# Optimization experiments

Measured on AMD Instinct MI355X. Metric: run time of the kernel, lower is better.

## Reference

```python
import jax, jax.numpy as jnp
import numpy as np

N = 50000
K = 32
C = 256  # hidden_dim

def setup_inputs() -> dict:
    key = jax.random.key(0)
    k1, k2, k3, k4 = jax.random.split(key, 4)
    feat = jax.random.normal(k1, (N, C), dtype=jnp.float32)
    coords = jax.random.normal(k2, (N, 3), dtype=jnp.float32)
    knn_idx = jax.random.randint(k3, (N, K), 0, N, dtype=jnp.int32)
    # Dense(hidden_dim) over concat([feat(C), agg(C), rel_mean(3), rel_std(3)]) -> in_dim = 2C + 6
    W = jax.random.normal(k4, (2 * C + 6, C), dtype=jnp.float32) * (1.0 / np.sqrt(2 * C + 6))
    b = jnp.zeros((C,), dtype=jnp.float32)
    return {"feat": feat, "coords": coords, "knn_idx": knn_idx, "W": W, "b": b}

def reference(feat, coords, knn_idx, W, b):
    # Neighbor feature aggregation: gather (N,K,C) then mean over K
    nbr_feat = feat[knn_idx]                      # (N, K, C)
    agg = jnp.mean(nbr_feat, axis=1)              # (N, C)
    # Relative coordinate statistics
    nbr_coords = coords[knn_idx]                  # (N, K, 3)
    rel = nbr_coords - coords[:, None, :]         # (N, K, 3)
    rel_mean = jnp.mean(rel, axis=1)              # (N, 3)
    rel_var = jnp.mean(jnp.square(rel), axis=1) - jnp.square(rel_mean)
    rel_std = jnp.sqrt(jnp.maximum(rel_var, 0.0))  # population std, like tf.math.reduce_std
    mix = jnp.concatenate([feat, agg, rel_mean, rel_std], axis=-1)  # (N, 2C+6)
    out = jax.nn.silu(mix @ W + b)                # (N, C)
    return out
```

## Files before the change

kernel.cpp:

```cpp
#include <hip/hip_runtime.h>
#include <math.h>


typedef __attribute__((ext_vector_type(8))) short short8;
typedef __attribute__((ext_vector_type(4))) float f32x4;
typedef __attribute__((ext_vector_type(2))) float f32x2;

constexpr int K = 32;
constexpr int C = 256;
constexpr int IN_DIM = 2 * C + 6;
constexpr int KP = 544;
constexpr int BM = 32;
constexpr int MIXS = 552;
constexpr int NT = 256;

__device__ __forceinline__ unsigned short f2bf(float f) {
  union { float f; unsigned u; } c; c.f = f;
  return (unsigned short)((c.u + 0x7fffu + ((c.u >> 16) & 1u)) >> 16);
}
__device__ __forceinline__ unsigned cvtpk(float lo, float hi) {
  unsigned r;
  asm("v_cvt_pk_bf16_f32 %0, %1, %2" : "=v"(r) : "v"(lo), "v"(hi));
  return r;
}

__global__ __launch_bounds__(256) void prep_feat_q(const float* __restrict__ feat,
                                                   uint2* __restrict__ featq,
                                                   long total8) {
  long i = (long)blockIdx.x * 256 + threadIdx.x;
  if (i < total8) {
    const float4 v0 = reinterpret_cast<const float4*>(feat)[2 * i];
    const float4 v1 = reinterpret_cast<const float4*>(feat)[2 * i + 1];
    unsigned a = 0, b = 0;
    a = __builtin_amdgcn_cvt_pk_fp8_f32(v0.x, v0.y, a, false);
    a = __builtin_amdgcn_cvt_pk_fp8_f32(v0.z, v0.w, a, true);
    b = __builtin_amdgcn_cvt_pk_fp8_f32(v1.x, v1.y, b, false);
    b = __builtin_amdgcn_cvt_pk_fp8_f32(v1.z, v1.w, b, true);
    uint2 o; o.x = a; o.y = b;
    featq[i] = o;
  }
}

__global__ __launch_bounds__(256) void prep_w(const float* __restrict__ W,
                                              unsigned short* __restrict__ Wt) {
  int i = blockIdx.x * 256 + threadIdx.x;
  if (i < C * KP) {
    int nn = i / KP, k = i - nn * KP;
    float v = (k < IN_DIM) ? W[(size_t)k * C + nn] : 0.f;
    if (k >= C && k < 2 * C) v *= (1.0f / 32.0f);
    Wt[i] = f2bf(v);
  }
}

__global__ __launch_bounds__(NT, 4)
void gcl_main(const unsigned char* __restrict__ featq,
              const float* __restrict__ feat,
              const float* __restrict__ coords,
              const int*   __restrict__ knn,
              const unsigned short* __restrict__ Wt,
              const float* __restrict__ bias,
              float* __restrict__ out, int n)
{
  __shared__ unsigned short mix[BM][MIXS];
  __shared__ int knnLds[BM * K];

  const int t = threadIdx.x;
  const int row0 = blockIdx.x * BM;

  #pragma unroll
  for (int i = 0; i < (BM * K) / NT; ++i) {
    int e = t + i * NT;
    int r = e >> 5, k = e & 31;
    int g = row0 + r; if (g >= n) g = n - 1;
    knnLds[e] = knn[(size_t)g * K + k];
  }
  for (int e = t; e < BM * (KP - IN_DIM); e += NT) {
    int r = e / (KP - IN_DIM), c = e - r * (KP - IN_DIM);
    mix[r][IN_DIM + c] = 0;
  }
  __syncthreads();

  const int w    = t >> 6;
  const int lane = t & 63;
  const int cl   = lane & 15;
  const int rq   = lane >> 4;

  #pragma unroll
  for (int p = 0; p < 2; ++p) {
    const int r = (w << 3) + (p << 2) + rq;
    int g = row0 + r; if (g >= n) g = n - 1;

    {
      const float4 s0 = *reinterpret_cast<const float4*>(feat + (size_t)g * C + cl * 16 + 0);
      const float4 s1 = *reinterpret_cast<const float4*>(feat + (size_t)g * C + cl * 16 + 4);
      const float4 s2 = *reinterpret_cast<const float4*>(feat + (size_t)g * C + cl * 16 + 8);
      const float4 s3 = *reinterpret_cast<const float4*>(feat + (size_t)g * C + cl * 16 + 12);
      uint4 o0, o1;
      o0.x = cvtpk(s0.x, s0.y); o0.y = cvtpk(s0.z, s0.w);
      o0.z = cvtpk(s1.x, s1.y); o0.w = cvtpk(s1.z, s1.w);
      o1.x = cvtpk(s2.x, s2.y); o1.y = cvtpk(s2.z, s2.w);
      o1.z = cvtpk(s3.x, s3.y); o1.w = cvtpk(s3.z, s3.w);
      *reinterpret_cast<uint4*>(&mix[r][cl * 16 + 0]) = o0;
      *reinterpret_cast<uint4*>(&mix[r][cl * 16 + 8]) = o1;
    }

    const int* ids = &knnLds[r * K];
    float a0=0,a1=0,a2=0,a3=0,a4=0,a5=0,a6=0,a7=0;
    float a8=0,a9=0,aA=0,aB=0,aC=0,aD=0,aE=0,aF=0;
    #pragma unroll 8
    for (int k = 0; k < K; ++k) {
      const uint4 v = *reinterpret_cast<const uint4*>(featq + (size_t)ids[k] * C + cl * 16);
      f32x2 d0 = __builtin_amdgcn_cvt_pk_f32_fp8(v.x, false);
      f32x2 d1 = __builtin_amdgcn_cvt_pk_f32_fp8(v.x, true);
      f32x2 d2 = __builtin_amdgcn_cvt_pk_f32_fp8(v.y, false);
      f32x2 d3 = __builtin_amdgcn_cvt_pk_f32_fp8(v.y, true);
      f32x2 d4 = __builtin_amdgcn_cvt_pk_f32_fp8(v.z, false);
      f32x2 d5 = __builtin_amdgcn_cvt_pk_f32_fp8(v.z, true);
      f32x2 d6 = __builtin_amdgcn_cvt_pk_f32_fp8(v.w, false);
      f32x2 d7 = __builtin_amdgcn_cvt_pk_f32_fp8(v.w, true);
      a0 += d0.x; a1 += d0.y; a2 += d1.x; a3 += d1.y;
      a4 += d2.x; a5 += d2.y; a6 += d3.x; a7 += d3.y;
      a8 += d4.x; a9 += d4.y; aA += d5.x; aB += d5.y;
      aC += d6.x; aD += d6.y; aE += d7.x; aF += d7.y;
    }
    uint4 o0, o1;
    o0.x = cvtpk(a0, a1); o0.y = cvtpk(a2, a3);
    o0.z = cvtpk(a4, a5); o0.w = cvtpk(a6, a7);
    o1.x = cvtpk(a8, a9); o1.y = cvtpk(aA, aB);
    o1.z = cvtpk(aC, aD); o1.w = cvtpk(aE, aF);
    *reinterpret_cast<uint4*>(&mix[r][C + cl * 16 + 0]) = o0;
    *reinterpret_cast<uint4*>(&mix[r][C + cl * 16 + 8]) = o1;
  }

  #pragma unroll
  for (int pass = 0; pass < 4; ++pass) {
    const int sr = (t >> 5) + pass * 8;
    const int sk = t & 31;
    const int id = knnLds[sr * K + sk];
    const float x = coords[(size_t)id * 3 + 0];
    const float y = coords[(size_t)id * 3 + 1];
    const float z = coords[(size_t)id * 3 + 2];
    float sx = x, sy = y, sz = z;
    float qx = x * x, qy = y * y, qz = z * z;
    #pragma unroll
    for (int m = 1; m < 32; m <<= 1) {
      sx += __shfl_xor(sx, m); sy += __shfl_xor(sy, m); sz += __shfl_xor(sz, m);
      qx += __shfl_xor(qx, m); qy += __shfl_xor(qy, m); qz += __shfl_xor(qz, m);
    }
    if (sk == 0) {
      int g = row0 + sr; if (g >= n) g = n - 1;
      const float inv = 1.0f / 32.0f;
      const float mx = sx * inv, my = sy * inv, mz = sz * inv;
      const float vx = qx * inv - mx * mx;
      const float vy = qy * inv - my * my;
      const float vz = qz * inv - mz * mz;
      mix[sr][2 * C + 0] = f2bf(mx - coords[(size_t)g * 3 + 0]);
      mix[sr][2 * C + 1] = f2bf(my - coords[(size_t)g * 3 + 1]);
      mix[sr][2 * C + 2] = f2bf(mz - coords[(size_t)g * 3 + 2]);
      mix[sr][2 * C + 3] = f2bf(sqrtf(fmaxf(vx, 0.f)));
      mix[sr][2 * C + 4] = f2bf(sqrtf(fmaxf(vy, 0.f)));
      mix[sr][2 * C + 5] = f2bf(sqrtf(fmaxf(vz, 0.f)));
    }
  }
  __syncthreads();

  const int n0  = w * 64;
  const int l15 = lane & 15;
  const int h   = lane >> 4;

  f32x4 acc[2][4];
  #pragma unroll
  for (int mt = 0; mt < 2; ++mt)
    #pragma unroll
    for (int nt = 0; nt < 4; ++nt)
      acc[mt][nt] = (f32x4){0.f, 0.f, 0.f, 0.f};

  const unsigned short* wb = Wt + (size_t)(n0 + l15) * KP + 8 * h;

  short8 B0 = *reinterpret_cast<const short8*>(wb + 0 * 16 * KP);
  short8 B1 = *reinterpret_cast<const short8*>(wb + 1 * 16 * KP);
  short8 B2 = *reinterpret_cast<const short8*>(wb + 2 * 16 * KP);
  short8 B3 = *reinterpret_cast<const short8*>(wb + 3 * 16 * KP);
  short8 A0 = *reinterpret_cast<const short8*>(&mix[l15][8 * h]);
  short8 A1 = *reinterpret_cast<const short8*>(&mix[16 + l15][8 * h]);

  #pragma unroll 1
  for (int s8 = 0; s8 < KP / 32; ++s8) {
    const int kb  = s8 * 32;
    const int kbn = (kb + 32 <= KP - 32) ? kb + 32 : KP - 32;
    short8 nB0 = *reinterpret_cast<const short8*>(wb + 0 * 16 * KP + kbn);
    short8 nB1 = *reinterpret_cast<const short8*>(wb + 1 * 16 * KP + kbn);
    short8 nB2 = *reinterpret_cast<const short8*>(wb + 2 * 16 * KP + kbn);
    short8 nB3 = *reinterpret_cast<const short8*>(wb + 3 * 16 * KP + kbn);
    short8 nA0 = *reinterpret_cast<const short8*>(&mix[l15][kbn + 8 * h]);
    short8 nA1 = *reinterpret_cast<const short8*>(&mix[16 + l15][kbn + 8 * h]);

    acc[0][0] = __builtin_amdgcn_mfma_f32_16x16x32_bf16(A0, B0, acc[0][0], 0, 0, 0);
    acc[1][0] = __builtin_amdgcn_mfma_f32_16x16x32_bf16(A1, B0, acc[1][0], 0, 0, 0);
    acc[0][1] = __builtin_amdgcn_mfma_f32_16x16x32_bf16(A0, B1, acc[0][1], 0, 0, 0);
    acc[1][1] = __builtin_amdgcn_mfma_f32_16x16x32_bf16(A1, B1, acc[1][1], 0, 0, 0);
    acc[0][2] = __builtin_amdgcn_mfma_f32_16x16x32_bf16(A0, B2, acc[0][2], 0, 0, 0);
    acc[1][2] = __builtin_amdgcn_mfma_f32_16x16x32_bf16(A1, B2, acc[1][2], 0, 0, 0);
    acc[0][3] = __builtin_amdgcn_mfma_f32_16x16x32_bf16(A0, B3, acc[0][3], 0, 0, 0);
    acc[1][3] = __builtin_amdgcn_mfma_f32_16x16x32_bf16(A1, B3, acc[1][3], 0, 0, 0);

    B0 = nB0; B1 = nB1; B2 = nB2; B3 = nB3;
    A0 = nA0; A1 = nA1;
  }

  #pragma unroll
  for (int mt = 0; mt < 2; ++mt) {
    #pragma unroll
    for (int nt = 0; nt < 4; ++nt) {
      const int col = n0 + nt * 16 + l15;
      const float bv = bias[col];
      f32x4 a = acc[mt][nt];
      #pragma unroll
      for (int q = 0; q < 4; ++q) {
        const int grow = row0 + mt * 16 + 4 * h + q;
        if (grow < n) {
          const float x = a[q] + bv;
          out[(size_t)grow * C + col] = x * __builtin_amdgcn_rcpf(1.f + __expf(-x));
        }
      }
    }
  }
}

constexpr int BMF = 32;
constexpr int MIX_STRIDE = 520;

#define FMA4(mcomp, wv)                                                        \
  a.x = fmaf((mcomp), (wv).x, a.x);                                            \
  a.y = fmaf((mcomp), (wv).y, a.y);                                            \
  a.z = fmaf((mcomp), (wv).z, a.z);                                            \
  a.w = fmaf((mcomp), (wv).w, a.w);

__global__ __launch_bounds__(256, 2)
void gcl_fused(const float* __restrict__ feat,
               const float* __restrict__ coords,
               const int*   __restrict__ knn,
               const float* __restrict__ W,
               const float* __restrict__ bias,
               float* __restrict__ out,
               int n)
{
  __shared__ float mix[BMF][MIX_STRIDE];
  __shared__ int   knnLds[BMF * K];

  const int t = threadIdx.x;
  const int row0 = blockIdx.x * BMF;

  #pragma unroll
  for (int i = 0; i < (BMF * K) / 256; ++i) {
    const int e = t + i * 256;
    const int r = e >> 5;
    const int k = e & (K - 1);
    int grow = row0 + r; if (grow >= n) grow = n - 1;
    knnLds[e] = knn[(size_t)grow * K + k];
  }
  __syncthreads();

  const int c4 = t & 63;
  const int rg = t >> 6;

  for (int ri = 0; ri < BMF / 4; ++ri) {
    const int r = rg * (BMF / 4) + ri;
    int grow = row0 + r; if (grow >= n) grow = n - 1;
    const int* ids = &knnLds[r * K];
    float sx = 0.f, sy = 0.f, sz = 0.f, sw = 0.f;
    #pragma unroll 8
    for (int k = 0; k < K; ++k) {
      const float4 f = *reinterpret_cast<const float4*>(feat + (size_t)ids[k] * C + c4 * 4);
      sx += f.x; sy += f.y; sz += f.z; sw += f.w;
    }
    const float4 self = *reinterpret_cast<const float4*>(feat + (size_t)grow * C + c4 * 4);
    float* mr = mix[r];
    *reinterpret_cast<float4*>(mr + c4 * 4) = self;
    const float inv = 1.0f / (float)K;
    float4 a; a.x = sx * inv; a.y = sy * inv; a.z = sz * inv; a.w = sw * inv;
    *reinterpret_cast<float4*>(mr + C + c4 * 4) = a;
  }

  if (t < BMF * 3) {
    const int r = t / 3;
    const int d = t - r * 3;
    int grow = row0 + r; if (grow >= n) grow = n - 1;
    const int* ids = &knnLds[r * K];
    float s = 0.f, ss = 0.f;
    #pragma unroll 8
    for (int k = 0; k < K; ++k) {
      const float v = coords[(size_t)ids[k] * 3 + d];
      s += v; ss += v * v;
    }
    const float inv = 1.0f / (float)K;
    const float m = s * inv;
    const float var = ss * inv - m * m;
    mix[r][2 * C + d]     = m - coords[(size_t)grow * 3 + d];
    mix[r][2 * C + 3 + d] = sqrtf(fmaxf(var, 0.f));
  }
  __syncthreads();

  const int c0 = (t & 63) * 4;
  const int rbase = rg * (BMF / 4);

  float4 acc[BMF / 4];
  {
    const float4 bv = *reinterpret_cast<const float4*>(bias + c0);
    #pragma unroll
    for (int ri = 0; ri < BMF / 4; ++ri) acc[ri] = bv;
  }

  for (int jb = 0; jb < 129; ++jb) {
    const int j = jb * 4;
    const float4 w0 = *reinterpret_cast<const float4*>(W + (size_t)(j + 0) * C + c0);
    const float4 w1 = *reinterpret_cast<const float4*>(W + (size_t)(j + 1) * C + c0);
    const float4 w2 = *reinterpret_cast<const float4*>(W + (size_t)(j + 2) * C + c0);
    const float4 w3 = *reinterpret_cast<const float4*>(W + (size_t)(j + 3) * C + c0);
    #pragma unroll
    for (int ri = 0; ri < BMF / 4; ++ri) {
      const float4 m4 = *reinterpret_cast<const float4*>(&mix[rbase + ri][j]);
      float4 a = acc[ri];
      FMA4(m4.x, w0)
      FMA4(m4.y, w1)
      FMA4(m4.z, w2)
      FMA4(m4.w, w3)
      acc[ri] = a;
    }
  }
  #pragma unroll
  for (int jt = IN_DIM - 2; jt < IN_DIM; ++jt) {
    const float4 wv = *reinterpret_cast<const float4*>(W + (size_t)jt * C + c0);
    #pragma unroll
    for (int ri = 0; ri < BMF / 4; ++ri) {
      const float m = mix[rbase + ri][jt];
      float4 a = acc[ri];
      FMA4(m, wv)
      acc[ri] = a;
    }
  }

  #pragma unroll
  for (int ri = 0; ri < BMF / 4; ++ri) {
    const int grow = row0 + rbase + ri;
    if (grow < n) {
      float4 a = acc[ri];
      a.x = a.x / (1.f + expf(-a.x));
      a.y = a.y / (1.f + expf(-a.y));
      a.z = a.z / (1.f + expf(-a.z));
      a.w = a.w / (1.f + expf(-a.w));
      *reinterpret_cast<float4*>(out + (size_t)grow * C + c0) = a;
    }
  }
}

extern "C" void kernel_launch(void* const* d_in, const int* in_sizes, int n_in,
                              void* d_out, int out_size, void* d_ws, size_t ws_size,
                              hipStream_t stream) {
  const float* feat   = (const float*)d_in[0];
  const float* coords = (const float*)d_in[1];
  const int*   knn    = (const int*)d_in[2];
  const float* W      = (const float*)d_in[3];
  const float* bias   = (const float*)d_in[4];
  float* out = (float*)d_out;

  const int n = in_sizes[0] / C;

  const size_t featq_bytes = (size_t)n * C;
  const size_t wt_bytes    = (size_t)C * KP * 2;

  if (ws_size >= featq_bytes + wt_bytes) {
    unsigned char* featq  = (unsigned char*)d_ws;
    unsigned short* Wt    = (unsigned short*)((char*)d_ws + featq_bytes);
    const long total8 = (long)n * C / 8;
    const int grid = (n + BM - 1) / BM;
    hipLaunchKernelGGL(prep_feat_q, dim3((unsigned)((total8 + 255) / 256)), dim3(256), 0, stream,
                       feat, (uint2*)featq, total8);
    hipLaunchKernelGGL(prep_w, dim3((C * KP + 255) / 256), dim3(256), 0, stream, W, Wt);
    hipLaunchKernelGGL(gcl_main, dim3(grid), dim3(NT), 0, stream,
                       featq, feat, coords, knn, Wt, bias, out, n);
  } else {
    const int gridf = (n + BMF - 1) / BMF;
    hipLaunchKernelGGL(gcl_fused, dim3(gridf), dim3(256), 0, stream,
                       feat, coords, knn, W, bias, out, n);
  }
}
```

Baseline: 124.9 us.

## Merge prep kernels, precompute bf16 feat copy and padded float4 coords

Replaces the two prep kernels with one launch that also writes a bf16 copy of feat and a float4-padded coords array. The main kernel then copies the self-feature row straight into LDS instead of reading fp32 and converting it. It also fetches each neighbor's coordinates with one 16-byte load instead of three scalar loads. The cost is extra prep work and workspace: a 25.6 MB bf16 write plus a 0.8 MB coords write, and the bf16 path is used only when the workspace is large enough.

```diff
diff --git a/kernel.cpp b/kernel.cpp
--- a/kernel.cpp
+++ b/kernel.cpp
@@ -24,42 +24,64 @@
   return r;
 }
 
-__global__ __launch_bounds__(256) void prep_feat_q(const float* __restrict__ feat,
-                                                   uint2* __restrict__ featq,
-                                                   long total8) {
-  long i = (long)blockIdx.x * 256 + threadIdx.x;
-  if (i < total8) {
-    const float4 v0 = reinterpret_cast<const float4*>(feat)[2 * i];
-    const float4 v1 = reinterpret_cast<const float4*>(feat)[2 * i + 1];
+__global__ __launch_bounds__(256)
+void prep_all(const float* __restrict__ feat,
+              const float* __restrict__ W,
+              const float* __restrict__ coords,
+              unsigned char*  __restrict__ featq,
+              unsigned short* __restrict__ featb,
+              unsigned short* __restrict__ Wt,
+              float4* __restrict__ coords4,
+              int n, int hasB)
+{
+  const long i  = (long)blockIdx.x * 256 + threadIdx.x;
+  const long nF = (long)n * 32;
+  const long nW = (long)C * KP;
+
+  if (i < nF) {
+    const int r = (int)(i >> 5), c8 = (int)(i & 31);
+    const int ch0 = c8 * 8;
+    const float4 v0 = *reinterpret_cast<const float4*>(feat + (size_t)r * C + ch0);
+    const float4 v1 = *reinterpret_cast<const float4*>(feat + (size_t)r * C + ch0 + 4);
     unsigned a = 0, b = 0;
     a = __builtin_amdgcn_cvt_pk_fp8_f32(v0.x, v0.y, a, false);
     a = __builtin_amdgcn_cvt_pk_fp8_f32(v0.z, v0.w, a, true);
     b = __builtin_amdgcn_cvt_pk_fp8_f32(v1.x, v1.y, b, false);
     b = __builtin_amdgcn_cvt_pk_fp8_f32(v1.z, v1.w, b, true);
-    uint2 o; o.x = a; o.y = b;
-    featq[i] = o;
-  }
-}
-
-__global__ __launch_bounds__(256) void prep_w(const float* __restrict__ W,
-                                              unsigned short* __restrict__ Wt) {
-  int i = blockIdx.x * 256 + threadIdx.x;
-  if (i < C * KP) {
-    int nn = i / KP, k = i - nn * KP;
+    uint2 oq; oq.x = a; oq.y = b;
+    *reinterpret_cast<uint2*>(featq + (size_t)r * C + ch0) = oq;
+    if (hasB) {
+      uint4 ob;
+      ob.x = cvtpk(v0.x, v0.y); ob.y = cvtpk(v0.z, v0.w);
+      ob.z = cvtpk(v1.x, v1.y); ob.w = cvtpk(v1.z, v1.w);
+      *reinterpret_cast<uint4*>(featb + (size_t)r * C + ch0) = ob;
+    }
+  } else if (i < nF + nW) {
+    const int j = (int)(i - nF);
+    const int nn = j / KP, k = j - nn * KP;
     float v = (k < IN_DIM) ? W[(size_t)k * C + nn] : 0.f;
     if (k >= C && k < 2 * C) v *= (1.0f / 32.0f);
-    Wt[i] = f2bf(v);
+    Wt[j] = f2bf(v);
+  } else if (i < nF + nW + n) {
+    const int r = (int)(i - nF - nW);
+    float4 o;
+    o.x = coords[(size_t)r * 3 + 0];
+    o.y = coords[(size_t)r * 3 + 1];
+    o.z = coords[(size_t)r * 3 + 2];
+    o.w = 0.f;
+    coords4[r] = o;
   }
 }
 
 __global__ __launch_bounds__(NT, 4)
 void gcl_main(const unsigned char* __restrict__ featq,
+              const unsigned short* __restrict__ featb,
               const float* __restrict__ feat,
-              const float* __restrict__ coords,
+              const float4* __restrict__ coords4,
               const int*   __restrict__ knn,
               const unsigned short* __restrict__ Wt,
               const float* __restrict__ bias,
-              float* __restrict__ out, int n)
+              float* __restrict__ out, int n, int hasB)
 {
   __shared__ unsigned short mix[BM][MIXS];
   __shared__ int knnLds[BM * K];
@@ -90,7 +112,13 @@
     const int r = (w << 3) + (p << 2) + rq;
     int g = row0 + r; if (g >= n) g = n - 1;
 
-    {
+    if (hasB) {
+      const unsigned short* fb = featb + (size_t)g * C + cl * 16;
+      *reinterpret_cast<uint4*>(&mix[r][cl * 16 + 0]) =
+          *reinterpret_cast<const uint4*>(fb);
+      *reinterpret_cast<uint4*>(&mix[r][cl * 16 + 8]) =
+          *reinterpret_cast<const uint4*>(fb + 8);
+    } else {
       const float4 s0 = *reinterpret_cast<const float4*>(feat + (size_t)g * C + cl * 16 + 0);
       const float4 s1 = *reinterpret_cast<const float4*>(feat + (size_t)g * C + cl * 16 + 4);
       const float4 s2 = *reinterpret_cast<const float4*>(feat + (size_t)g * C + cl * 16 + 8);
@@ -137,11 +165,9 @@
     const int sr = (t >> 5) + pass * 8;
     const int sk = t & 31;
     const int id = knnLds[sr * K + sk];
-    const float x = coords[(size_t)id * 3 + 0];
-    const float y = coords[(size_t)id * 3 + 1];
-    const float z = coords[(size_t)id * 3 + 2];
-    float sx = x, sy = y, sz = z;
-    float qx = x * x, qy = y * y, qz = z * z;
+    const float4 cv = coords4[id];
+    float sx = cv.x, sy = cv.y, sz = cv.z;
+    float qx = cv.x * cv.x, qy = cv.y * cv.y, qz = cv.z * cv.z;
     #pragma unroll
     for (int m = 1; m < 32; m <<= 1) {
       sx += __shfl_xor(sx, m); sy += __shfl_xor(sy, m); sz += __shfl_xor(sz, m);
@@ -149,14 +175,15 @@
     }
     if (sk == 0) {
       int g = row0 + sr; if (g >= n) g = n - 1;
+      const float4 cc = coords4[g];
       const float inv = 1.0f / 32.0f;
       const float mx = sx * inv, my = sy * inv, mz = sz * inv;
       const float vx = qx * inv - mx * mx;
       const float vy = qy * inv - my * my;
       const float vz = qz * inv - mz * mz;
-      mix[sr][2 * C + 0] = f2bf(mx - coords[(size_t)g * 3 + 0]);
-      mix[sr][2 * C + 1] = f2bf(my - coords[(size_t)g * 3 + 1]);
-      mix[sr][2 * C + 2] = f2bf(mz - coords[(size_t)g * 3 + 2]);
+      mix[sr][2 * C + 0] = f2bf(mx - cc.x);
+      mix[sr][2 * C + 1] = f2bf(my - cc.y);
+      mix[sr][2 * C + 2] = f2bf(mz - cc.z);
       mix[sr][2 * C + 3] = f2bf(sqrtf(fmaxf(vx, 0.f)));
       mix[sr][2 * C + 4] = f2bf(sqrtf(fmaxf(vy, 0.f)));
       mix[sr][2 * C + 5] = f2bf(sqrtf(fmaxf(vz, 0.f)));
@@ -366,19 +393,30 @@
 
   const int n = in_sizes[0] / C;
 
-  const size_t featq_bytes = (size_t)n * C;
-  const size_t wt_bytes    = (size_t)C * KP * 2;
-
-  if (ws_size >= featq_bytes + wt_bytes) {
-    unsigned char* featq  = (unsigned char*)d_ws;
-    unsigned short* Wt    = (unsigned short*)((char*)d_ws + featq_bytes);
-    const long total8 = (long)n * C / 8;
+  const size_t featq_b  = (size_t)n * C;
+  const size_t featb_b  = (size_t)n * C * 2;
+  const size_t wt_b     = (size_t)C * KP * 2;
+  const size_t coords_b = (size_t)n * 16;
+  const size_t need1 = featq_b + featb_b + wt_b + coords_b;
+  const size_t need2 = featq_b + wt_b + coords_b;
+
+  if (ws_size >= need2) {
+    const int hasB = (ws_size >= need1) ? 1 : 0;
+    char* p = (char*)d_ws;
+    unsigned char*  featq = (unsigned char*)p;              p += featq_b;
+    unsigned short* featb = nullptr;
+    if (hasB) { featb = (unsigned short*)p;                 p += featb_b; }
+    unsigned short* Wt    = (unsigned short*)p;             p += wt_b;
+    float4*         c4    = (float4*)p;
+
+    const long totalPrep = (long)n * 32 + (long)C * KP + n;
+    const int gridP = (int)((totalPrep + 255) / 256);
+    hipLaunchKernelGGL(prep_all, dim3(gridP), dim3(256), 0, stream,
+                       feat, W, coords, featq, featb, Wt, c4, n, hasB);
+
     const int grid = (n + BM - 1) / BM;
-    hipLaunchKernelGGL(prep_feat_q, dim3((unsigned)((total8 + 255) / 256)), dim3(256), 0, stream,
-                       feat, (uint2*)featq, total8);
-    hipLaunchKernelGGL(prep_w, dim3((C * KP + 255) / 256), dim3(256), 0, stream, W, Wt);
     hipLaunchKernelGGL(gcl_main, dim3(grid), dim3(NT), 0, stream,
-                       featq, feat, coords, knn, Wt, bias, out, n);
+                       featq, featb, feat, c4, knn, Wt, bias, out, n, hasB);
   } else {
     const int gridf = (n + BMF - 1) / BMF;
     hipLaunchKernelGGL(gcl_fused, dim3(gridf), dim3(256), 0, stream,
```

Result: no change. 125.1 us (+0.2%).
